# Kernel tuning notes

Hardware: AMD Instinct MI355X
Metric: run time of the kernel (lower is better)

## Reference

```python
import jax, jax.numpy as jnp
import numpy as np


def setup_inputs() -> dict:
    key = jax.random.key(0)
    k1, k2 = jax.random.split(key)
    node_num = 10000
    n_edges = 640000
    d = 128
    embs = jax.random.normal(k1, (node_num, d), dtype=jnp.float32)
    ratings = jax.random.randint(k2, (n_edges, 2), 0, node_num, dtype=jnp.int32)
    return {"embs": embs, "ratings": ratings, "node_num": node_num}


def reference(embs, ratings, node_num):
    # edge endpoints: row (source) and column (neighbor) indices
    r0 = ratings[:, 0]
    r1 = ratings[:, 1]
    # edge dot-product attention scores  [E]
    scores = jnp.sum(embs[r0] * embs[r1], axis=-1)
    # sparse row-wise softmax (torch.sparse.softmax over dim=1)
    seg_max = jax.ops.segment_max(scores, r0, num_segments=node_num)
    seg_max = jnp.where(jnp.isfinite(seg_max), seg_max, jnp.float32(0.0))  # empty rows
    ex = jnp.exp(scores - seg_max[r0])
    denom = jax.ops.segment_sum(ex, r0, num_segments=node_num)
    attn = ex / denom[r0]
    # attention weights are detached in the original module
    attn = jax.lax.stop_gradient(attn)
    # sparse mm aggregation: out[i] = sum_{e: r0[e]=i} attn[e] * embs[r1[e]]
    out = jax.ops.segment_sum(attn[:, None] * embs[r1], r0, num_segments=node_num)
    return out
```

## Files before the change

### kernel.cpp

```cpp
#include <hip/hip_runtime.h>
#include <hip/hip_bf16.h>
#include <math.h>


#define K_CHUNKS 256
#define NODE_LDS 10240
#define NPAD 10240
#define STAGE_LDS 2560
#define EXP_CLAMP 80.0f
#define MAXE_W 128

__global__ __launch_bounds__(1024) void build_kernel(const int2* __restrict__ ratings,
                             unsigned short* __restrict__ mtmp,
                             unsigned short* __restrict__ staging,
                             int n_edges, int node_num, int chunk_size) {
    __shared__ int hist[NODE_LDS];
    __shared__ unsigned short stage[STAGE_LDS];
    __shared__ int lds_ws[16];
    __shared__ int lds_wp[16];

    int tid  = threadIdx.x;
    int lane = tid & 63;
    int wid  = tid >> 6;
    int k    = blockIdx.x;

    for (int i = tid; i < NODE_LDS; i += 1024) hist[i] = 0;
    __syncthreads();

    int base = k * chunk_size;
    int end  = base + chunk_size; if (end > n_edges) end = n_edges;

    for (int e = base + tid; e < end; e += 1024)
        atomicAdd(&hist[ratings[e].x], 1);
    __syncthreads();

    const int B = NODE_LDS / 1024;
    int b0 = tid * B;
    int c[B];
    int local = 0;
    #pragma unroll
    for (int j = 0; j < B; ++j) {
        c[j] = hist[b0 + j];
        local += c[j];
    }
    int incl = local;
    #pragma unroll
    for (int off = 1; off < 64; off <<= 1) {
        int t = __shfl_up(incl, off, 64);
        if (lane >= off) incl += t;
    }
    if (lane == 63) lds_ws[wid] = incl;
    __syncthreads();
    if (wid == 0 && lane < 16) {
        int wv = lds_ws[lane];
        #pragma unroll
        for (int off = 1; off < 16; off <<= 1) {
            int t = __shfl_up(wv, off, 64);
            if (lane >= off) wv += t;
        }
        lds_wp[lane] = wv;
    }
    __syncthreads();
    int run = ((wid > 0) ? lds_wp[wid - 1] : 0) + (incl - local);

    unsigned short* mrow = mtmp + (size_t)k * NPAD;
    #pragma unroll
    for (int j = 0; j < B; ++j) {
        int i = b0 + j;
        int cc = (c[j] > 15) ? 15 : c[j];
        mrow[i] = (unsigned short)(((unsigned int)run << 4) | (unsigned int)cc);
        hist[i] = run;
        run += c[j];
    }
    __syncthreads();

    for (int e = base + tid; e < end; e += 1024) {
        int2 r = ratings[e];
        int pos = atomicAdd(&hist[r.x], 1);
        if (pos < STAGE_LDS) stage[pos] = (unsigned short)r.y;
    }
    __syncthreads();

    int nsh = end - base;
    unsigned int* g  = (unsigned int*)(staging + (size_t)k * chunk_size);
    unsigned int* sg = (unsigned int*)stage;
    int nu = (nsh + 1) >> 1;
    for (int i = tid; i < nu; i += 1024) g[i] = sg[i];
}

__global__ __launch_bounds__(256) void transpose_kernel(const unsigned short* __restrict__ mtmp,
                                                        unsigned short* __restrict__ meta_t,
                                                        int node_num) {
    __shared__ unsigned short tile[64][66];
    int n0 = blockIdx.x * 64;
    int k0 = blockIdx.y * 64;
    int tx = threadIdx.x & 63;
    int ty = threadIdx.x >> 6;
    #pragma unroll
    for (int r = 0; r < 64; r += 4) {
        int n = n0 + tx;
        tile[r + ty][tx] = (n < node_num) ? mtmp[(size_t)(k0 + r + ty) * NPAD + n] : 0;
    }
    __syncthreads();
    #pragma unroll
    for (int r = 0; r < 64; r += 4) {
        int n = n0 + r + ty;
        if (n < node_num)
            meta_t[(size_t)n * K_CHUNKS + k0 + tx] = tile[tx][r + ty];
    }
}

__global__ __launch_bounds__(256) void node_kernel(const float* __restrict__ embs,
                            const unsigned short* __restrict__ meta_t,
                            const unsigned short* __restrict__ staging,
                            float* __restrict__ out,
                            int node_num, int chunk_size) {
    __shared__ int    s_r1[4][MAXE_W];
    __shared__ float4 s_acc[2][2][16];
    __shared__ float  s_l[2];

    int tid   = threadIdx.x;
    int lane  = tid & 63;
    int wid   = tid >> 6;
    int slot  = wid >> 1;
    int w     = wid & 1;
    int g     = lane >> 4;
    int t     = lane & 15;
    int n     = blockIdx.x * 2 + slot;
    bool nvalid = (n < node_num);
    int nc    = nvalid ? n : 0;

    const unsigned int* mrow32 = (const unsigned int*)(meta_t + (size_t)nc * K_CHUNKS);
    unsigned int mm = nvalid ? mrow32[w * 64 + lane] : 0u;
    unsigned int e0 = mm & 0xffffu, e1 = mm >> 16;
    int c0 = (int)(e0 & 15u), o0 = (int)(e0 >> 4);
    int c1 = (int)(e1 & 15u), o1 = (int)(e1 >> 4);
    int cnt = c0 + c1;
    int incl = cnt;
    #pragma unroll
    for (int off = 1; off < 64; off <<= 1) {
        int tt = __shfl_up(incl, off, 64);
        if (lane >= off) incl += tt;
    }
    int basep = incl - cnt;
    int E = __shfl(incl, 63, 64);
    if (E > MAXE_W) E = MAXE_W;
    {
        int k0 = w * 128 + lane * 2;
        int idx = basep;
        const unsigned short* s0 = staging + (size_t)k0 * chunk_size + o0;
        for (int q = 0; q < c0; ++q) {
            if (idx < MAXE_W) s_r1[wid][idx] = (int)s0[q];
            ++idx;
        }
        const unsigned short* s1 = staging + (size_t)(k0 + 1) * chunk_size + o1;
        for (int q = 0; q < c1; ++q) {
            if (idx < MAXE_W) s_r1[wid][idx] = (int)s1[q];
            ++idx;
        }
    }

    const float4* row_n = (const float4*)(embs + (size_t)nc * 128);
    float4 av0 = row_n[t];
    float4 av1 = row_n[16 + t];

    float  l = 0.f;
    float4 acc0 = make_float4(0.f, 0.f, 0.f, 0.f);
    float4 acc1 = make_float4(0.f, 0.f, 0.f, 0.f);

    for (int base = 0; base < E; base += 16) {
        bool  valid[4];
        int   r1[4];
        #pragma unroll
        for (int b = 0; b < 4; ++b) {
            int idx = base + b * 4 + g;
            valid[b] = (idx < E);
            r1[b] = valid[b] ? s_r1[wid][idx] : 0;
        }
        float4 v0[4], v1[4];
        #pragma unroll
        for (int b = 0; b < 4; ++b) {
            const float4* row = (const float4*)(embs + (size_t)r1[b] * 128);
            v0[b] = row[t];
            v1[b] = row[16 + t];
        }
        float s[4];
        #pragma unroll
        for (int b = 0; b < 4; ++b) {
            float d = v0[b].x * av0.x;
            d = fmaf(v0[b].y, av0.y, d);
            d = fmaf(v0[b].z, av0.z, d);
            d = fmaf(v0[b].w, av0.w, d);
            d = fmaf(v1[b].x, av1.x, d);
            d = fmaf(v1[b].y, av1.y, d);
            d = fmaf(v1[b].z, av1.z, d);
            d = fmaf(v1[b].w, av1.w, d);
            s[b] = d;
        }
        #pragma unroll
        for (int b = 0; b < 4; ++b) {
            #pragma unroll
            for (int off = 1; off < 16; off <<= 1)
                s[b] += __shfl_xor(s[b], off, 64);
        }
        float p[4];
        #pragma unroll
        for (int b = 0; b < 4; ++b)
            p[b] = valid[b] ? __expf(fminf(s[b], EXP_CLAMP)) : 0.f;
        l += (p[0] + p[1]) + (p[2] + p[3]);
        #pragma unroll
        for (int b = 0; b < 4; ++b) {
            acc0.x = fmaf(p[b], v0[b].x, acc0.x);
            acc0.y = fmaf(p[b], v0[b].y, acc0.y);
            acc0.z = fmaf(p[b], v0[b].z, acc0.z);
            acc0.w = fmaf(p[b], v0[b].w, acc0.w);
            acc1.x = fmaf(p[b], v1[b].x, acc1.x);
            acc1.y = fmaf(p[b], v1[b].y, acc1.y);
            acc1.z = fmaf(p[b], v1[b].z, acc1.z);
            acc1.w = fmaf(p[b], v1[b].w, acc1.w);
        }
    }

    #pragma unroll
    for (int off = 16; off <= 32; off <<= 1) {
        l      += __shfl_xor(l,      off, 64);
        acc0.x += __shfl_xor(acc0.x, off, 64);
        acc0.y += __shfl_xor(acc0.y, off, 64);
        acc0.z += __shfl_xor(acc0.z, off, 64);
        acc0.w += __shfl_xor(acc0.w, off, 64);
        acc1.x += __shfl_xor(acc1.x, off, 64);
        acc1.y += __shfl_xor(acc1.y, off, 64);
        acc1.z += __shfl_xor(acc1.z, off, 64);
        acc1.w += __shfl_xor(acc1.w, off, 64);
    }

    if (w == 1 && g == 0) {
        s_acc[slot][0][t] = acc0;
        s_acc[slot][1][t] = acc1;
        if (lane == 0) s_l[slot] = l;
    }
    __syncthreads();
    if (w == 0 && g == 0 && nvalid) {
        float4 b0 = s_acc[slot][0][t];
        float4 b1 = s_acc[slot][1][t];
        float L = l + s_l[slot];
        float inv = (L > 0.f) ? 1.f / L : 0.f;
        float4* orow = (float4*)(out + (size_t)n * 128);
        orow[t]      = make_float4((acc0.x + b0.x) * inv, (acc0.y + b0.y) * inv,
                                   (acc0.z + b0.z) * inv, (acc0.w + b0.w) * inv);
        orow[16 + t] = make_float4((acc1.x + b1.x) * inv, (acc1.y + b1.y) * inv,
                                   (acc1.z + b1.z) * inv, (acc1.w + b1.w) * inv);
    }
}

extern "C" void kernel_launch(void* const* d_in, const int* in_sizes, int n_in,
                              void* d_out, int out_size, void* d_ws, size_t ws_size,
                              hipStream_t stream) {
    const float* embs    = (const float*)d_in[0];
    const int*   ratings = (const int*)d_in[1];
    const int d        = 128;
    const int node_num = in_sizes[0] / d;
    const int n_edges  = in_sizes[1] / 2;
    float* out = (float*)d_out;

    int chunk_size = (n_edges + K_CHUNKS - 1) / K_CHUNKS;
    if (chunk_size & 1) chunk_size += 1;

    auto align256 = [](size_t x) { return (x + 255) & ~(size_t)255; };
    char* ws = (char*)d_ws;
    unsigned short* mtmp = (unsigned short*)ws;
    ws += align256((size_t)K_CHUNKS * NPAD * 2);
    unsigned short* meta_t = (unsigned short*)ws;
    ws += align256((size_t)node_num * K_CHUNKS * 2);
    unsigned short* staging = (unsigned short*)ws;
    ws += align256((size_t)K_CHUNKS * chunk_size * 2);

    build_kernel<<<K_CHUNKS, 1024, 0, stream>>>(
        (const int2*)ratings, mtmp, staging, n_edges, node_num, chunk_size);

    {
        dim3 grid((node_num + 63) / 64, K_CHUNKS / 64);
        transpose_kernel<<<grid, 256, 0, stream>>>(mtmp, meta_t, node_num);
    }

    {
        int blocks = (node_num + 1) / 2;
        node_kernel<<<blocks, 256, 0, stream>>>(embs, meta_t, staging, out, node_num, chunk_size);
    }
}
```

Measured before the change: 101.0 us.

## Gather neighbor embeddings as fp16 copy and cache edge loads in build

Adds an fp32-to-fp16 conversion of the embedding table, fused into the transpose kernel, and has the node kernel gather neighbor rows from that half-size copy, widening it back to fp32 for the dot products and accumulation. The aim is to halve the bytes moved by the random row gathers. In exchange the scores and outputs lose precision, and every call adds a conversion pass over the whole table. The build kernel also keeps its first three edges per thread in registers, so the second scatter pass does not read them from global memory again.

```diff
diff --git a/kernel.cpp b/kernel.cpp
--- a/kernel.cpp
+++ b/kernel.cpp
@@ -1,5 +1,6 @@
 #include <hip/hip_runtime.h>
 #include <hip/hip_bf16.h>
+#include <hip/hip_fp16.h>
 #include <math.h>
 
 
@@ -30,7 +31,16 @@
     int base = k * chunk_size;
     int end  = base + chunk_size; if (end > n_edges) end = n_edges;
 
-    for (int e = base + tid; e < end; e += 1024)
+    int e0i = base + tid, e1i = e0i + 1024, e2i = e1i + 1024;
+    bool h0 = e0i < end, h1 = e1i < end, h2 = e2i < end;
+    int2 r0v = h0 ? ratings[e0i] : make_int2(0, 0);
+    int2 r1v = h1 ? ratings[e1i] : make_int2(0, 0);
+    int2 r2v = h2 ? ratings[e2i] : make_int2(0, 0);
+
+    if (h0) atomicAdd(&hist[r0v.x], 1);
+    if (h1) atomicAdd(&hist[r1v.x], 1);
+    if (h2) atomicAdd(&hist[r2v.x], 1);
+    for (int e = base + 3072 + tid; e < end; e += 1024)
         atomicAdd(&hist[ratings[e].x], 1);
     __syncthreads();
 
@@ -74,10 +84,13 @@
     }
     __syncthreads();
 
-    for (int e = base + tid; e < end; e += 1024) {
+    if (h0) { int p = atomicAdd(&hist[r0v.x], 1); if (p < STAGE_LDS) stage[p] = (unsigned short)r0v.y; }
+    if (h1) { int p = atomicAdd(&hist[r1v.x], 1); if (p < STAGE_LDS) stage[p] = (unsigned short)r1v.y; }
+    if (h2) { int p = atomicAdd(&hist[r2v.x], 1); if (p < STAGE_LDS) stage[p] = (unsigned short)r2v.y; }
+    for (int e = base + 3072 + tid; e < end; e += 1024) {
         int2 r = ratings[e];
-        int pos = atomicAdd(&hist[r.x], 1);
-        if (pos < STAGE_LDS) stage[pos] = (unsigned short)r.y;
+        int p = atomicAdd(&hist[r.x], 1);
+        if (p < STAGE_LDS) stage[p] = (unsigned short)r.y;
     }
     __syncthreads();
 
@@ -90,6 +103,8 @@
 
 __global__ __launch_bounds__(256) void transpose_kernel(const unsigned short* __restrict__ mtmp,
                                                         unsigned short* __restrict__ meta_t,
+                                                        const float4* __restrict__ embs4,
+                                                        ushort4* __restrict__ embs16,
                                                         int node_num) {
     __shared__ unsigned short tile[64][66];
     int n0 = blockIdx.x * 64;
@@ -108,9 +123,28 @@
         if (n < node_num)
             meta_t[(size_t)n * K_CHUNKS + k0 + tx] = tile[tx][r + ty];
     }
+
+    int nblocks = gridDim.x * gridDim.y;
+    int bid = blockIdx.y * gridDim.x + blockIdx.x;
+    int nf4 = node_num * 32;
+    int per = (nf4 + nblocks - 1) / nblocks;
+    int s0 = bid * per;
+    int s1 = s0 + per; if (s1 > nf4) s1 = nf4;
+    for (int i = s0 + (int)threadIdx.x; i < s1; i += 256) {
+        float4 v = embs4[i];
+        __half hx = __float2half(v.x), hy = __float2half(v.y);
+        __half hz = __float2half(v.z), hw = __float2half(v.w);
+        ushort4 o;
+        o.x = *reinterpret_cast<unsigned short*>(&hx);
+        o.y = *reinterpret_cast<unsigned short*>(&hy);
+        o.z = *reinterpret_cast<unsigned short*>(&hz);
+        o.w = *reinterpret_cast<unsigned short*>(&hw);
+        embs16[i] = o;
+    }
 }
 
 __global__ __launch_bounds__(256) void node_kernel(const float* __restrict__ embs,
+                            const unsigned short* __restrict__ embs16,
                             const unsigned short* __restrict__ meta_t,
                             const unsigned short* __restrict__ staging,
                             float* __restrict__ out,
@@ -160,9 +194,9 @@
         }
     }
 
-    const float4* row_n = (const float4*)(embs + (size_t)nc * 128);
-    float4 av0 = row_n[t];
-    float4 av1 = row_n[16 + t];
+    const float4* arow = (const float4*)(embs + (size_t)nc * 128);
+    float4 av0 = arow[2 * t];
+    float4 av1 = arow[2 * t + 1];
 
     float  l = 0.f;
     float4 acc0 = make_float4(0.f, 0.f, 0.f, 0.f);
@@ -177,24 +211,34 @@
             valid[b] = (idx < E);
             r1[b] = valid[b] ? s_r1[wid][idx] : 0;
         }
-        float4 v0[4], v1[4];
-        #pragma unroll
-        for (int b = 0; b < 4; ++b) {
-            const float4* row = (const float4*)(embs + (size_t)r1[b] * 128);
-            v0[b] = row[t];
-            v1[b] = row[16 + t];
+        uint4 u[4];
+        #pragma unroll
+        for (int b = 0; b < 4; ++b)
+            u[b] = ((const uint4*)(embs16 + (size_t)r1[b] * 128))[t];
+        float v[4][8];
+        #pragma unroll
+        for (int b = 0; b < 4; ++b) {
+            const __half2* hp = reinterpret_cast<const __half2*>(&u[b]);
+            float2 f0 = __half22float2(hp[0]);
+            float2 f1 = __half22float2(hp[1]);
+            float2 f2 = __half22float2(hp[2]);
+            float2 f3 = __half22float2(hp[3]);
+            v[b][0] = f0.x; v[b][1] = f0.y;
+            v[b][2] = f1.x; v[b][3] = f1.y;
+            v[b][4] = f2.x; v[b][5] = f2.y;
+            v[b][6] = f3.x; v[b][7] = f3.y;
         }
         float s[4];
         #pragma unroll
         for (int b = 0; b < 4; ++b) {
-            float d = v0[b].x * av0.x;
-            d = fmaf(v0[b].y, av0.y, d);
-            d = fmaf(v0[b].z, av0.z, d);
-            d = fmaf(v0[b].w, av0.w, d);
-            d = fmaf(v1[b].x, av1.x, d);
-            d = fmaf(v1[b].y, av1.y, d);
-            d = fmaf(v1[b].z, av1.z, d);
-            d = fmaf(v1[b].w, av1.w, d);
+            float d = v[b][0] * av0.x;
+            d = fmaf(v[b][1], av0.y, d);
+            d = fmaf(v[b][2], av0.z, d);
+            d = fmaf(v[b][3], av0.w, d);
+            d = fmaf(v[b][4], av1.x, d);
+            d = fmaf(v[b][5], av1.y, d);
+            d = fmaf(v[b][6], av1.z, d);
+            d = fmaf(v[b][7], av1.w, d);
             s[b] = d;
         }
         #pragma unroll
@@ -210,14 +254,14 @@
         l += (p[0] + p[1]) + (p[2] + p[3]);
         #pragma unroll
         for (int b = 0; b < 4; ++b) {
-            acc0.x = fmaf(p[b], v0[b].x, acc0.x);
-            acc0.y = fmaf(p[b], v0[b].y, acc0.y);
-            acc0.z = fmaf(p[b], v0[b].z, acc0.z);
-            acc0.w = fmaf(p[b], v0[b].w, acc0.w);
-            acc1.x = fmaf(p[b], v1[b].x, acc1.x);
-            acc1.y = fmaf(p[b], v1[b].y, acc1.y);
-            acc1.z = fmaf(p[b], v1[b].z, acc1.z);
-            acc1.w = fmaf(p[b], v1[b].w, acc1.w);
+            acc0.x = fmaf(p[b], v[b][0], acc0.x);
+            acc0.y = fmaf(p[b], v[b][1], acc0.y);
+            acc0.z = fmaf(p[b], v[b][2], acc0.z);
+            acc0.w = fmaf(p[b], v[b][3], acc0.w);
+            acc1.x = fmaf(p[b], v[b][4], acc1.x);
+            acc1.y = fmaf(p[b], v[b][5], acc1.y);
+            acc1.z = fmaf(p[b], v[b][6], acc1.z);
+            acc1.w = fmaf(p[b], v[b][7], acc1.w);
         }
     }
 
@@ -246,10 +290,10 @@
         float L = l + s_l[slot];
         float inv = (L > 0.f) ? 1.f / L : 0.f;
         float4* orow = (float4*)(out + (size_t)n * 128);
-        orow[t]      = make_float4((acc0.x + b0.x) * inv, (acc0.y + b0.y) * inv,
-                                   (acc0.z + b0.z) * inv, (acc0.w + b0.w) * inv);
-        orow[16 + t] = make_float4((acc1.x + b1.x) * inv, (acc1.y + b1.y) * inv,
-                                   (acc1.z + b1.z) * inv, (acc1.w + b1.w) * inv);
+        orow[2 * t]     = make_float4((acc0.x + b0.x) * inv, (acc0.y + b0.y) * inv,
+                                      (acc0.z + b0.z) * inv, (acc0.w + b0.w) * inv);
+        orow[2 * t + 1] = make_float4((acc1.x + b1.x) * inv, (acc1.y + b1.y) * inv,
+                                      (acc1.z + b1.z) * inv, (acc1.w + b1.w) * inv);
     }
 }
 
@@ -274,17 +318,21 @@
     ws += align256((size_t)node_num * K_CHUNKS * 2);
     unsigned short* staging = (unsigned short*)ws;
     ws += align256((size_t)K_CHUNKS * chunk_size * 2);
+    unsigned short* embs16 = (unsigned short*)ws;
+    ws += align256((size_t)node_num * 128 * 2);
 
     build_kernel<<<K_CHUNKS, 1024, 0, stream>>>(
         (const int2*)ratings, mtmp, staging, n_edges, node_num, chunk_size);
 
     {
         dim3 grid((node_num + 63) / 64, K_CHUNKS / 64);
-        transpose_kernel<<<grid, 256, 0, stream>>>(mtmp, meta_t, node_num);
+        transpose_kernel<<<grid, 256, 0, stream>>>(
+            mtmp, meta_t, (const float4*)embs, (ushort4*)embs16, node_num);
     }
 
     {
         int blocks = (node_num + 1) / 2;
-        node_kernel<<<blocks, 256, 0, stream>>>(embs, meta_t, staging, out, node_num, chunk_size);
+        node_kernel<<<blocks, 256, 0, stream>>>(
+            embs, embs16, meta_t, staging, out, node_num, chunk_size);
     }
 }
```

Result: no change. 100.9 us (-0.0%).
